# Kernel optimization log

Measured on AMD Instinct MI355X. Metric: run time of the kernel, lower is better.

Reference implementation:

```python
import jax, jax.numpy as jnp
import numpy as np

N = 50000      # nodes
E = 800000     # edges
H = 128        # hidden_features
EF = 8         # edge_features (before distance concat)
L = 2          # num_layers
NF = 100.0     # normalization_factor
NC = 1.0       # norm_constant
ATTN = True
USE_TANH = False
TANH_RANGE = 15.0
EIN = 2 * H + EF + 1  # GCL / coord-MLP edge input dim


def setup_inputs() -> dict:
    key = jax.random.key(0)
    ks = jax.random.split(key, 16)
    s = 0.02
    w = lambda k, shape: (jax.random.normal(k, shape, jnp.float32) * s)
    return dict(
        x=jax.random.normal(ks[0], (N, H), jnp.float32),
        pos=jax.random.normal(ks[1], (N, 3), jnp.float32),
        mask=jnp.ones((N, 1), jnp.float32),
        edge_attr=jax.random.normal(ks[2], (E, EF), jnp.float32),
        edge_index=jax.random.randint(ks[3], (2, E), 0, N),
        # GCL layer params, stacked over L layers
        W_e1=w(ks[4], (L, EIN, H)), b_e1=jnp.zeros((L, H), jnp.float32),
        W_e2=w(ks[5], (L, H, H)),  b_e2=jnp.zeros((L, H), jnp.float32),
        W_att=w(ks[6], (L, H, 1)), b_att=jnp.zeros((L, 1), jnp.float32),
        W_n1=w(ks[7], (L, 2 * H, H)), b_n1=jnp.zeros((L, H), jnp.float32),
        W_n2=w(ks[8], (L, H, H)),  b_n2=jnp.zeros((L, H), jnp.float32),
        # Equivariant coordinate-update MLP (last layer has no bias)
        cW1=w(ks[9], (EIN, H)), cb1=jnp.zeros((H,), jnp.float32),
        cW2=w(ks[10], (H, H)), cb2=jnp.zeros((H,), jnp.float32),
        cW3=w(ks[11], (H, 1)),
    )


def reference(x, pos, mask, edge_attr, edge_index,
              W_e1, b_e1, W_e2, b_e2, W_att, b_att, W_n1, b_n1, W_n2, b_n2,
              cW1, cb1, cW2, cb2, cW3):
    silu = jax.nn.silu
    row, col = edge_index[0], edge_index[1]  # aggregate messages at row
    diff = pos[row] - pos[col]                         # [E, 3]
    d2 = jnp.sum(diff * diff, axis=-1, keepdims=True)  # [E, 1] squared distance
    ea = jnp.concatenate([d2, edge_attr], axis=-1)     # [E, EF+1]

    # GCL message-passing layers (residual node update)
    for l in range(L):
        he = jnp.concatenate([x[row], x[col], ea], axis=-1)   # [E, EIN]
        m = silu(silu(he @ W_e1[l] + b_e1[l]) @ W_e2[l] + b_e2[l])
        if ATTN:
            m = m * jax.nn.sigmoid(m @ W_att[l] + b_att[l])
        agg = jax.ops.segment_sum(m, row, num_segments=N) / NF
        x = x + silu(jnp.concatenate([x, agg], axis=-1) @ W_n1[l] + b_n1[l]) @ W_n2[l] + b_n2[l]

    # Equivariant coordinate update
    he = jnp.concatenate([x[row], x[col], ea], axis=-1)
    phi = silu(silu(he @ cW1 + cb1) @ cW2 + cb2) @ cW3        # [E, 1]
    if USE_TANH:
        phi = jnp.tanh(phi) * TANH_RANGE
    nd = diff / (jnp.sqrt(d2) + NC)                           # normalized direction
    trans = nd * phi                                          # [E, 3]
    pos = pos + (jax.ops.segment_sum(trans, row, num_segments=N) / NF) * mask
    return (x, pos)
```

## Files before the change

kernel.cpp:

```cpp
#include <hip/hip_runtime.h>
#include <hip/hip_bf16.h>
#include <stdint.h>

#define NN 50000
#define NE 800000
#define HH 128

typedef __bf16 bf16x8 __attribute__((ext_vector_type(8)));
typedef float  f32x4  __attribute__((ext_vector_type(4)));
typedef long   f8frag;

__device__ __forceinline__ unsigned short f2bf(float f) {
  union { float f; uint32_t u; } v; v.f = f;
  uint32_t r = v.u + 0x7FFFu + ((v.u >> 16) & 1u);
  return (unsigned short)(r >> 16);
}
__device__ __forceinline__ float b2f(unsigned short u) {
  union { float f; uint32_t u; } v; v.u = (uint32_t)u << 16; return v.f;
}
#if __has_builtin(__builtin_amdgcn_cvt_pk_bf16_f32)
typedef __bf16 bf16x2 __attribute__((ext_vector_type(2)));
__device__ __forceinline__ uint32_t pack2bf(float a, float b) {
  union { bf16x2 v; uint32_t u; } t;
  t.v = __builtin_amdgcn_cvt_pk_bf16_f32(a, b);
  return t.u;
}
#else
__device__ __forceinline__ uint32_t pack2bf(float a, float b) {
  return (uint32_t)f2bf(a) | ((uint32_t)f2bf(b) << 16);
}
#endif
__device__ __forceinline__ uint8_t f2fp8(float v) {
  return (uint8_t)(__builtin_amdgcn_cvt_pk_fp8_f32(v, 0.f, 0, false) & 0xff);
}
__device__ __forceinline__ float silu_f(float x) {
  return x * __builtin_amdgcn_rcpf(1.f + __expf(-x));
}
__device__ __forceinline__ float sigm_f(float x) {
  return __builtin_amdgcn_rcpf(1.f + __expf(-x));
}

__device__ __forceinline__ bf16x8 frag_ld(const short* blk, int row, int q) {
  int c = q ^ ((row >> 1) & 3);
  return *(const bf16x8*)(blk + row * 32 + c * 8);
}
__device__ __forceinline__ int wfrag_off(int row, int q) {
  return row * 32 + ((q ^ ((row >> 1) & 3)) * 8);
}
__device__ __forceinline__ bf16x8 fragf32(const float* src, float sc) {
  float4 lo = *(const float4*)src;
  float4 hi = *(const float4*)(src + 4);
  union { uint32_t u[4]; bf16x8 v; } t;
  t.u[0] = pack2bf(lo.x * sc, lo.y * sc);
  t.u[1] = pack2bf(lo.z * sc, lo.w * sc);
  t.u[2] = pack2bf(hi.x * sc, hi.y * sc);
  t.u[3] = pack2bf(hi.z * sc, hi.w * sc);
  return t.v;
}

__global__ void k_prep_weights(const float* We1, const float* We2, const float* Wn1,
                               const float* Wn2, const float* cW1, const float* cW2,
                               uint8_t* W1f8, short* W2sw, short* Wn1sw, short* Wn2sw,
                               short* W1csw) {
  int idx = blockIdx.x * 256 + threadIdx.x;
  if (idx < 110592) {
    int l = idx / 36864, rem = idx % 36864;
    const float* s = (l == 0) ? We1 : (l == 1) ? We1 + 33920 : cW1;
    int kkb = rem >> 12, r2 = rem & 4095;
    int n = r2 >> 5, kw = r2 & 31;
    int k = kkb * 32 + kw;
    float v = (k < 265) ? s[k * 128 + n] : 0.f;
    W1f8[idx] = f2fp8(v);
    return;
  }
  idx -= 110592;
  if (idx < 49152) {
    int l = idx >> 14, rem = idx & 16383;
    const float* s = (l == 0) ? We2 : (l == 1) ? We2 + 16384 : cW2;
    int kkb = rem >> 12, r2 = rem & 4095, n = r2 >> 5, kw = r2 & 31;
    int cp = kw >> 3, j = kw & 7, c = cp ^ ((n >> 1) & 3);
    int k = kkb * 32 + c * 8 + j;
    W2sw[(l << 14) + (rem)] = (short)f2bf(s[k * 128 + n]);
    return;
  }
  idx -= 49152;
  if (idx < 65536) {
    int l = idx >> 15, rem = idx & 32767;
    const float* s = Wn1 + l * 32768;
    int kkb = rem >> 12, r2 = rem & 4095, n = r2 >> 5, kw = r2 & 31;
    int cp = kw >> 3, j = kw & 7, c = cp ^ ((n >> 1) & 3);
    int k = kkb * 32 + c * 8 + j;
    Wn1sw[(l << 15) + rem] = (short)f2bf(s[k * 128 + n]);
    return;
  }
  idx -= 65536;
  if (idx < 32768) {
    int l = idx >> 14, rem = idx & 16383;
    const float* s = Wn2 + l * 16384;
    int kkb = rem >> 12, r2 = rem & 4095, n = r2 >> 5, kw = r2 & 31;
    int cp = kw >> 3, j = kw & 7, c = cp ^ ((n >> 1) & 3);
    int k = kkb * 32 + c * 8 + j;
    Wn2sw[(l << 14) + rem] = (short)f2bf(s[k * 128 + n]);
    return;
  }
  idx -= 32768;
  if (idx < 98304) {
    int l = idx / 32768, rem = idx % 32768;
    const float* s = (l == 0) ? We1 : (l == 1) ? We1 + 33920 : cW1;
    int kkb = rem >> 13, r2 = rem & 8191, n = r2 >> 5, kw = r2 & 31;
    int cp = kw >> 3, j = kw & 7, c = cp ^ ((n >> 1) & 3);
    int k = kkb * 32 + c * 8 + j;
    float v = (n < 128) ? s[k * 128 + n] : s[(128 + k) * 128 + (n - 128)];
    W1csw[l * 32768 + rem] = (short)f2bf(v);
  }
}

__global__ void k_edge_pre(const float* __restrict__ pos, const float* __restrict__ eattr,
                           const int* __restrict__ ei, const int* __restrict__ inv,
                           int* __restrict__ rowS, int* __restrict__ colS,
                           uint8_t* __restrict__ eaF8, float* __restrict__ ndS) {
  int e = blockIdx.x * 256 + threadIdx.x;
  if (e >= NE) return;
  int r = ei[e], c = ei[NE + e];
  float dx = pos[r * 3 + 0] - pos[c * 3 + 0];
  float dy = pos[r * 3 + 1] - pos[c * 3 + 1];
  float dz = pos[r * 3 + 2] - pos[c * 3 + 2];
  float d2 = dx * dx + dy * dy + dz * dz;
  float invd = __builtin_amdgcn_rcpf(sqrtf(d2) + 1.f);
  int p = inv[e];
  rowS[p] = r;
  colS[p] = c;
  ndS[p * 3 + 0] = dx * invd;
  ndS[p * 3 + 1] = dy * invd;
  ndS[p * 3 + 2] = dz * invd;
  const float* ea = eattr + (size_t)e * 8;
  uint32_t w0 = __builtin_amdgcn_cvt_pk_fp8_f32(d2, ea[0], 0, false);
  w0 = __builtin_amdgcn_cvt_pk_fp8_f32(ea[1], ea[2], w0, true);
  uint32_t w1 = __builtin_amdgcn_cvt_pk_fp8_f32(ea[3], ea[4], 0, false);
  w1 = __builtin_amdgcn_cvt_pk_fp8_f32(ea[5], ea[6], w1, true);
  uint32_t w2 = __builtin_amdgcn_cvt_pk_fp8_f32(ea[7], 0.f, 0, false);
  uint4 v = {w0, w1, w2, 0u};
  *(uint4*)(eaF8 + (size_t)p * 16) = v;
}
__global__ void k_pos_final(const float* __restrict__ pos, const float* __restrict__ mask,
                            const float* __restrict__ pagg, float* __restrict__ out) {
  int i = blockIdx.x * 256 + threadIdx.x;
  if (i < NN * 3) out[i] = pos[i] + pagg[i] * 0.01f * mask[i / 3];
}

__global__ void k_hist(const int* __restrict__ ei, int* __restrict__ cnt) {
  int e = blockIdx.x * 256 + threadIdx.x;
  if (e < NE) atomicAdd(&cnt[ei[e]], 1);
}
__global__ void k_scan_block(const int* __restrict__ cnt, int* __restrict__ offs,
                             int* __restrict__ bsum) {
  __shared__ int s[256];
  int i = blockIdx.x * 256 + threadIdx.x;
  int v = (i < NN) ? cnt[i] : 0;
  s[threadIdx.x] = v;
  __syncthreads();
#pragma unroll
  for (int d = 1; d < 256; d <<= 1) {
    int t = (threadIdx.x >= d) ? s[threadIdx.x - d] : 0;
    __syncthreads();
    s[threadIdx.x] += t;
    __syncthreads();
  }
  if (i < NN) offs[i] = s[threadIdx.x] - v;
  if (threadIdx.x == 255) bsum[blockIdx.x] = s[255];
}
__global__ void k_scan_top(int* __restrict__ bsum) {
  __shared__ int s[256];
  int v = (threadIdx.x < 196) ? bsum[threadIdx.x] : 0;
  s[threadIdx.x] = v;
  __syncthreads();
#pragma unroll
  for (int d = 1; d < 256; d <<= 1) {
    int t = (threadIdx.x >= d) ? s[threadIdx.x - d] : 0;
    __syncthreads();
    s[threadIdx.x] += t;
    __syncthreads();
  }
  if (threadIdx.x < 196) bsum[threadIdx.x] = s[threadIdx.x] - v;
}
__global__ void k_scan_add(int* __restrict__ offs, const int* __restrict__ bsum) {
  int i = blockIdx.x * 256 + threadIdx.x;
  if (i < NN) offs[i] += bsum[blockIdx.x];
}
__global__ void k_scatter(const int* __restrict__ ei, int* __restrict__ offs,
                          int* __restrict__ inv) {
  int e = blockIdx.x * 256 + threadIdx.x;
  if (e < NE) inv[e] = atomicAdd(&offs[ei[e]], 1);
}

__global__ __launch_bounds__(256) void k_h1(
    const float* __restrict__ x, const short* __restrict__ W1c,
    const float* __restrict__ b1, short* __restrict__ H1RC) {
  const int tid = threadIdx.x, lane = tid & 63, w = tid >> 6;
  const int ln = lane & 15, q = lane >> 4;
  const int tile = blockIdx.x;
  size_t nbase[4];
  int wofs[4];
#pragma unroll
  for (int i = 0; i < 4; ++i) {
    int node = tile * 64 + i * 16 + ln;
    nbase[i] = (size_t)(node < NN ? node : (NN - 1)) * 128;
    int row = w * 64 + i * 16 + ln;
    wofs[i] = row * 32 + ((q ^ ((row >> 1) & 3)) * 8);
  }
  f32x4 acc[4][4];
  const f32x4 zero4 = {0.f, 0.f, 0.f, 0.f};
#pragma unroll
  for (int mi = 0; mi < 4; ++mi)
#pragma unroll
    for (int ni = 0; ni < 4; ++ni) acc[mi][ni] = zero4;
#pragma unroll
  for (int kk = 0; kk < 4; ++kk) {
    bf16x8 af[4], bfr[4];
#pragma unroll
    for (int i = 0; i < 4; ++i) af[i] = fragf32(x + nbase[i] + kk * 32 + q * 8, 1.f);
#pragma unroll
    for (int i = 0; i < 4; ++i) bfr[i] = *(const bf16x8*)(W1c + kk * 8192 + wofs[i]);
#pragma unroll
    for (int mi = 0; mi < 4; ++mi)
#pragma unroll
      for (int ni = 0; ni < 4; ++ni)
        acc[mi][ni] = __builtin_amdgcn_mfma_f32_16x16x32_bf16(af[mi], bfr[ni], acc[mi][ni], 0, 0, 0);
  }
  float b1v[4];
#pragma unroll
  for (int ni = 0; ni < 4; ++ni) {
    int ch = w * 64 + ni * 16 + ln;
    b1v[ni] = (ch < 128) ? b1[ch] : 0.f;
  }
#pragma unroll
  for (int mi = 0; mi < 4; ++mi)
#pragma unroll
    for (int r = 0; r < 4; ++r) {
      int node = tile * 64 + mi * 16 + q * 4 + r;
      if (node < NN) {
        ushort4 pk;
        pk.x = f2bf(acc[mi][0][r] + b1v[0]);
        pk.y = f2bf(acc[mi][1][r] + b1v[1]);
        pk.z = f2bf(acc[mi][2][r] + b1v[2]);
        pk.w = f2bf(acc[mi][3][r] + b1v[3]);
        *(ushort4*)(H1RC + (size_t)node * 256 + w * 64 + ln * 4) = pk;
      }
    }
}

template <int COORD>
__global__ __launch_bounds__(256, 4) void k_edge_gemm(
    const short* __restrict__ H1RC, const uint8_t* __restrict__ eaF8,
    const int* __restrict__ rowS, const int* __restrict__ colS,
    const uint8_t* __restrict__ W1f8, const short* __restrict__ W2l,
    const float* __restrict__ b2,
    const float* __restrict__ wred, const float* __restrict__ batt,
    const float* __restrict__ ndS, float* outAcc) {
  __shared__ __align__(16) short A2s[8192];
  __shared__ float redp[64][2];
  __shared__ __align__(16) unsigned short attb[64];
  __shared__ int srow[64];
  __shared__ __align__(8) unsigned char srunS[64];
  __shared__ int runrowS[64];
  __shared__ int cntS[1];

  const int tid = threadIdx.x;
  const int lane = tid & 63;
  const int w = tid >> 6;
  const int ln = lane & 15, q = lane >> 4;
  const int wm = w >> 1, wn = w & 1;

  const int nwg = gridDim.x;
  const int qq = nwg >> 3, rr = nwg & 7;
  const int xcd = blockIdx.x & 7, bidx = blockIdx.x >> 3;
  const int tile = (xcd < rr ? xcd * (qq + 1) : rr * (qq + 1) + (xcd - rr) * qq) + bidx;

  if (tid < 64) srow[tid] = rowS[tile * 64 + tid];
  __syncthreads();

  bool is_start = (tid < 64) && (tid == 0 || srow[tid] != srow[tid - 1]);
  unsigned long long bmask = __ballot(is_start);
  if (tid == 0) cntS[0] = __popcll(bmask);
  if (tid < 64) {
    int run = __popcll(bmask & ((1ull << lane) - 1ull)) + (is_start ? 1 : 0) - 1;
    srunS[tid] = (unsigned char)run;
    if (is_start) runrowS[run] = srow[tid];
  }

  const int e0 = wm * 32 + ln, e1 = e0 + 16;
  const uint32_t cbp = (uint32_t)(wn * 64 + q * 16);
  const uint32_t hr0 = (uint32_t)srow[e0] * 256u + cbp;
  const uint32_t hr1 = (uint32_t)srow[e1] * 256u + cbp;
  const uint32_t hc0 = (uint32_t)colS[tile * 64 + e0] * 256u + 128u + cbp;
  const uint32_t hc1 = (uint32_t)colS[tile * 64 + e1] * 256u + 128u + cbp;
  const uint32_t ea0 = (uint32_t)(tile * 64 + e0) * 16u + (uint32_t)((q & 1) * 8);
  const uint32_t ea1 = (uint32_t)(tile * 64 + e1) * 16u + (uint32_t)((q & 1) * 8);
  int wofs8[4], wofs[4];
#pragma unroll
  for (int i = 0; i < 4; ++i) {
    wofs8[i] = (wn * 64 + i * 16 + ln) * 32 + q * 8;
    wofs[i] = wfrag_off(wn * 64 + i * 16 + ln, q);
  }

  union U8 { uint4 v; unsigned short s[8]; };
  U8 xr[2][2], xc[2][2];
  xr[0][0].v = *(const uint4*)(H1RC + hr0);
  xr[0][1].v = *(const uint4*)(H1RC + hr0 + 8);
  xr[1][0].v = *(const uint4*)(H1RC + hr1);
  xr[1][1].v = *(const uint4*)(H1RC + hr1 + 8);
  xc[0][0].v = *(const uint4*)(H1RC + hc0);
  xc[0][1].v = *(const uint4*)(H1RC + hc0 + 8);
  xc[1][0].v = *(const uint4*)(H1RC + hc1);
  xc[1][1].v = *(const uint4*)(H1RC + hc1 + 8);

  f32x4 acc[4][2];
  const f32x4 zero4 = {0.f, 0.f, 0.f, 0.f};
#pragma unroll
  for (int ni = 0; ni < 4; ++ni)
#pragma unroll
    for (int mi = 0; mi < 2; ++mi) acc[ni][mi] = zero4;

  {
    const uint8_t* W1ea = W1f8 + 8 * 4096;
    f8frag wf[4], hf[2];
#pragma unroll
    for (int i = 0; i < 4; ++i) wf[i] = *(const f8frag*)(W1ea + wofs8[i]);
    hf[0] = (q < 2) ? *(const f8frag*)(eaF8 + ea0) : 0L;
    hf[1] = (q < 2) ? *(const f8frag*)(eaF8 + ea1) : 0L;
#pragma unroll
    for (int ni = 0; ni < 4; ++ni)
#pragma unroll
      for (int mi = 0; mi < 2; ++mi)
        acc[ni][mi] = __builtin_amdgcn_mfma_f32_16x16x32_fp8_fp8(wf[ni], hf[mi], acc[ni][mi], 0, 0, 0);
  }

#pragma unroll
  for (int ni = 0; ni < 4; ++ni) {
    int cb = wn * 64 + ni * 16 + q * 4;
    int kkb = cb >> 5, cc = (cb >> 3) & 3, j0 = cb & 7;
#pragma unroll
    for (int mi = 0; mi < 2; ++mi) {
      int edge = wm * 32 + mi * 16 + ln;
      int addr = kkb * 2048 + edge * 32 + ((cc ^ ((edge >> 1) & 3)) * 8) + j0;
      float h0 = silu_f(acc[ni][mi][0] + b2f(xr[mi][0].s[ni]) + b2f(xc[mi][0].s[ni]));
      float h1 = silu_f(acc[ni][mi][1] + b2f(xr[mi][0].s[4 + ni]) + b2f(xc[mi][0].s[4 + ni]));
      float h2 = silu_f(acc[ni][mi][2] + b2f(xr[mi][1].s[ni]) + b2f(xc[mi][1].s[ni]));
      float h3 = silu_f(acc[ni][mi][3] + b2f(xr[mi][1].s[4 + ni]) + b2f(xc[mi][1].s[4 + ni]));
      uint2 pk;
      pk.x = pack2bf(h0, h1);
      pk.y = pack2bf(h2, h3);
      *(uint2*)(A2s + addr) = pk;
    }
  }
  __syncthreads();

  f32x4 acc2[4][2];
#pragma unroll
  for (int ni = 0; ni < 4; ++ni)
#pragma unroll
    for (int mi = 0; mi < 2; ++mi) acc2[ni][mi] = zero4;
#pragma unroll
  for (int kk = 0; kk < 4; ++kk) {
    bf16x8 wf[4], hf[2];
#pragma unroll
    for (int i = 0; i < 4; ++i) wf[i] = *(const bf16x8*)(W2l + kk * 4096 + wofs[i]);
#pragma unroll
    for (int i = 0; i < 2; ++i) hf[i] = frag_ld(A2s + kk * 2048, wm * 32 + i * 16 + ln, q);
#pragma unroll
    for (int ni = 0; ni < 4; ++ni)
#pragma unroll
      for (int mi = 0; mi < 2; ++mi)
        acc2[ni][mi] = __builtin_amdgcn_mfma_f32_16x16x32_bf16(wf[ni], hf[mi], acc2[ni][mi], 0, 0, 0);
  }

  float4 b2v[4], wv[4];
#pragma unroll
  for (int ni = 0; ni < 4; ++ni) {
    b2v[ni] = *(const float4*)(b2 + wn * 64 + ni * 16 + q * 4);
    wv[ni]  = *(const float4*)(wred + wn * 64 + ni * 16 + q * 4);
  }
  float p[2] = {0.f, 0.f};
#pragma unroll
  for (int ni = 0; ni < 4; ++ni)
#pragma unroll
    for (int mi = 0; mi < 2; ++mi)
#pragma unroll
      for (int r = 0; r < 4; ++r) {
        float v = silu_f(acc2[ni][mi][r] + ((const float*)&b2v[ni])[r]);
        acc2[ni][mi][r] = v;
        p[mi] += v * ((const float*)&wv[ni])[r];
      }
#pragma unroll
  for (int mi = 0; mi < 2; ++mi) {
    p[mi] += __shfl_xor(p[mi], 16, 64);
    p[mi] += __shfl_xor(p[mi], 32, 64);
  }
  if (lane < 16) {
#pragma unroll
    for (int mi = 0; mi < 2; ++mi) redp[wm * 32 + mi * 16 + ln][wn] = p[mi];
  }
  __syncthreads();

  if (COORD == 0) {
    if (tid < 64) attb[tid] = f2bf(sigm_f(redp[tid][0] + redp[tid][1] + batt[0]));
#pragma unroll
    for (int ni = 0; ni < 4; ++ni)
#pragma unroll
      for (int mi = 0; mi < 2; ++mi) {
        int eb = mi * 16 + ln;
        int cE = (eb >> 3) & 3, jE = eb & 7;
#pragma unroll
        for (int r = 0; r < 4; ++r) {
          int chan2 = wn * 64 + ni * 16 + q * 4 + r;
          int addr = wm * 4096 + chan2 * 32 + ((cE ^ ((chan2 >> 1) & 3)) * 8) + jE;
          union { float f; uint32_t u; } vv;
          vv.f = acc2[ni][mi][r];
          A2s[addr] = (short)((vv.u + 0x8000u) >> 16);
        }
      }
    __syncthreads();
    const int nruns = cntS[0];
    bf16x8 bfrg[2][2];
#pragma unroll
    for (int kk = 0; kk < 2; ++kk)
#pragma unroll
      for (int ni = 0; ni < 2; ++ni)
        bfrg[kk][ni] = frag_ld(A2s + kk * 4096, w * 32 + ni * 16 + ln, q);
    const int npass = (nruns + 15) >> 4;
    for (int pp = 0; pp < npass; ++pp) {
      const unsigned int base = pp * 16;
      f32x4 a3c[2] = {zero4, zero4};
#pragma unroll
      for (int kk = 0; kk < 2; ++kk) {
        uint2 sb = *(const uint2*)(srunS + kk * 32 + q * 8);
        U8 ab;
        ab.v = *(const uint4*)(attb + kk * 32 + q * 8);
        union { short s[8]; bf16x8 v; } af;
#pragma unroll
        for (int j = 0; j < 4; ++j)
          af.s[j] = (((sb.x >> (8 * j)) & 255u) == base + (unsigned)ln) ? (short)ab.s[j] : (short)0;
#pragma unroll
        for (int j = 0; j < 4; ++j)
          af.s[4 + j] = (((sb.y >> (8 * j)) & 255u) == base + (unsigned)ln) ? (short)ab.s[4 + j] : (short)0;
        a3c[0] = __builtin_amdgcn_mfma_f32_16x16x32_bf16(af.v, bfrg[kk][0], a3c[0], 0, 0, 0);
        a3c[1] = __builtin_amdgcn_mfma_f32_16x16x32_bf16(af.v, bfrg[kk][1], a3c[1], 0, 0, 0);
      }
#pragma unroll
      for (int ni = 0; ni < 2; ++ni)
#pragma unroll
        for (int r = 0; r < 4; ++r) {
          int run = (int)base + q * 4 + r;
          if (run < nruns) {
            int rw = runrowS[run];
            atomicAdd(&outAcc[(size_t)rw * 128 + (w * 32 + ni * 16 + ln)], a3c[ni][r]);
          }
        }
    }
  } else {
    float* ndl = (float*)A2s;
    if (tid < 64) {
      float phi = redp[tid][0] + redp[tid][1];
      ndl[tid * 3 + 0] = ndS[(size_t)(tile * 64 + tid) * 3 + 0] * phi;
      ndl[tid * 3 + 1] = ndS[(size_t)(tile * 64 + tid) * 3 + 1] * phi;
      ndl[tid * 3 + 2] = ndS[(size_t)(tile * 64 + tid) * 3 + 2] * phi;
    }
    __syncthreads();
    if (is_start) {
      int myrow = srow[tid];
      float s0 = 0.f, s1 = 0.f, s2 = 0.f;
      for (int j = tid; j < 64 && srow[j] == myrow; ++j) {
        s0 += ndl[j * 3 + 0];
        s1 += ndl[j * 3 + 1];
        s2 += ndl[j * 3 + 2];
      }
      atomicAdd(&outAcc[myrow * 3 + 0], s0);
      atomicAdd(&outAcc[myrow * 3 + 1], s1);
      atomicAdd(&outAcc[myrow * 3 + 2], s2);
    }
  }
}

__global__ __launch_bounds__(256) void k_node_gemm(
    const float* __restrict__ agg,
    const short* __restrict__ Wn1l, const short* __restrict__ Wn2l,
    const float* __restrict__ b1, const float* __restrict__ b2,
    const float* __restrict__ xres, float* __restrict__ xout,
    const short* __restrict__ W1cN, const float* __restrict__ b1N,
    short* __restrict__ H1RC) {
  __shared__ short A2s[4 * 2048];

  const int tid = threadIdx.x;
  const int lane = tid & 63;
  const int w = tid >> 6;
  const int ln = lane & 15, q = lane >> 4;
  const int wm = w >> 1, wn = w & 1;
  const int tile = blockIdx.x;

  size_t nbase[2];
  int wofs[4];
#pragma unroll
  for (int i = 0; i < 2; ++i) {
    int node = tile * 64 + wm * 32 + i * 16 + ln;
    nbase[i] = (size_t)(node < NN ? node : (NN - 1)) * 128;
  }
#pragma unroll
  for (int i = 0; i < 4; ++i) wofs[i] = wfrag_off(wn * 64 + i * 16 + ln, q);

  f32x4 acc[2][4];
  const f32x4 zero4 = {0.f, 0.f, 0.f, 0.f};
#pragma unroll
  for (int mi = 0; mi < 2; ++mi)
#pragma unroll
    for (int ni = 0; ni < 4; ++ni) acc[mi][ni] = zero4;

#pragma unroll
  for (int kk = 0; kk < 8; ++kk) {
    bf16x8 af[2], bfr[4];
#pragma unroll
    for (int i = 0; i < 2; ++i) {
      if (kk < 4) af[i] = fragf32(xres + nbase[i] + kk * 32 + q * 8, 1.f);
      else        af[i] = fragf32(agg + nbase[i] + (kk - 4) * 32 + q * 8, 0.01f);
    }
#pragma unroll
    for (int i = 0; i < 4; ++i) bfr[i] = *(const bf16x8*)(Wn1l + kk * 4096 + wofs[i]);
#pragma unroll
    for (int mi = 0; mi < 2; ++mi)
#pragma unroll
      for (int ni = 0; ni < 4; ++ni)
        acc[mi][ni] = __builtin_amdgcn_mfma_f32_16x16x32_bf16(af[mi], bfr[ni], acc[mi][ni], 0, 0, 0);
  }

  float b1v[4];
#pragma unroll
  for (int ni = 0; ni < 4; ++ni) b1v[ni] = b1[wn * 64 + ni * 16 + ln];
#pragma unroll
  for (int mi = 0; mi < 2; ++mi)
#pragma unroll
    for (int ni = 0; ni < 4; ++ni) {
      int chan = wn * 64 + ni * 16 + ln;
      int kkb = chan >> 5, c = (chan >> 3) & 3, jj = chan & 7;
#pragma unroll
      for (int r = 0; r < 4; ++r) {
        int m = wm * 32 + mi * 16 + q * 4 + r;
        float v = silu_f(acc[mi][ni][r] + b1v[ni]);
        A2s[kkb * 2048 + m * 32 + ((c ^ ((m >> 1) & 3)) * 8) + jj] = (short)f2bf(v);
      }
    }
  __syncthreads();

  f32x4 acc2[2][4];
#pragma unroll
  for (int mi = 0; mi < 2; ++mi)
#pragma unroll
    for (int ni = 0; ni < 4; ++ni) acc2[mi][ni] = zero4;
#pragma unroll
  for (int kk = 0; kk < 4; ++kk) {
    bf16x8 af[2], bfr[4];
#pragma unroll
    for (int i = 0; i < 2; ++i) af[i] = frag_ld(A2s + kk * 2048, wm * 32 + i * 16 + ln, q);
#pragma unroll
    for (int i = 0; i < 4; ++i) bfr[i] = *(const bf16x8*)(Wn2l + kk * 4096 + wofs[i]);
#pragma unroll
    for (int mi = 0; mi < 2; ++mi)
#pragma unroll
      for (int ni = 0; ni < 4; ++ni)
        acc2[mi][ni] = __builtin_amdgcn_mfma_f32_16x16x32_bf16(af[mi], bfr[ni], acc2[mi][ni], 0, 0, 0);
  }

  float b2v[4];
#pragma unroll
  for (int ni = 0; ni < 4; ++ni) b2v[ni] = b2[wn * 64 + ni * 16 + ln];
#pragma unroll
  for (int mi = 0; mi < 2; ++mi)
#pragma unroll
    for (int r = 0; r < 4; ++r) {
      int m = wm * 32 + mi * 16 + q * 4 + r;
      int node = tile * 64 + m;
      if (node < NN) {
#pragma unroll
        for (int ni = 0; ni < 4; ++ni) {
          int chan = wn * 64 + ni * 16 + ln;
          float v = acc2[mi][ni][r] + b2v[ni] + xres[(size_t)node * 128 + chan];
          acc2[mi][ni][r] = v;
          xout[(size_t)node * 128 + chan] = v;
        }
      }
    }

  __syncthreads();
#pragma unroll
  for (int mi = 0; mi < 2; ++mi)
#pragma unroll
    for (int ni = 0; ni < 4; ++ni) {
      int chan = wn * 64 + ni * 16 + ln;
      int kkb = chan >> 5, c = (chan >> 3) & 3, jj = chan & 7;
#pragma unroll
      for (int r = 0; r < 4; ++r) {
        int m = wm * 32 + mi * 16 + q * 4 + r;
        A2s[kkb * 2048 + m * 32 + ((c ^ ((m >> 1) & 3)) * 8) + jj] = (short)f2bf(acc2[mi][ni][r]);
      }
    }
  __syncthreads();

  int wofsH[4];
#pragma unroll
  for (int i = 0; i < 4; ++i) {
    int row = w * 64 + i * 16 + ln;
    wofsH[i] = row * 32 + ((q ^ ((row >> 1) & 3)) * 8);
  }
  f32x4 acc3[4][4];
#pragma unroll
  for (int mi = 0; mi < 4; ++mi)
#pragma unroll
    for (int ni = 0; ni < 4; ++ni) acc3[mi][ni] = zero4;
#pragma unroll
  for (int kk = 0; kk < 4; ++kk) {
    bf16x8 af[4], bfr[4];
#pragma unroll
    for (int i = 0; i < 4; ++i) af[i] = frag_ld(A2s + kk * 2048, i * 16 + ln, q);
#pragma unroll
    for (int i = 0; i < 4; ++i) bfr[i] = *(const bf16x8*)(W1cN + kk * 8192 + wofsH[i]);
#pragma unroll
    for (int mi = 0; mi < 4; ++mi)
#pragma unroll
      for (int ni = 0; ni < 4; ++ni)
        acc3[mi][ni] = __builtin_amdgcn_mfma_f32_16x16x32_bf16(af[mi], bfr[ni], acc3[mi][ni], 0, 0, 0);
  }
  float b1v2[4];
#pragma unroll
  for (int ni = 0; ni < 4; ++ni) {
    int ch = w * 64 + ni * 16 + ln;
    b1v2[ni] = (ch < 128) ? b1N[ch] : 0.f;
  }
#pragma unroll
  for (int mi = 0; mi < 4; ++mi)
#pragma unroll
    for (int r = 0; r < 4; ++r) {
      int node = tile * 64 + mi * 16 + q * 4 + r;
      if (node < NN) {
        ushort4 pk;
        pk.x = f2bf(acc3[mi][0][r] + b1v2[0]);
        pk.y = f2bf(acc3[mi][1][r] + b1v2[1]);
        pk.z = f2bf(acc3[mi][2][r] + b1v2[2]);
        pk.w = f2bf(acc3[mi][3][r] + b1v2[3]);
        *(ushort4*)(H1RC + (size_t)node * 256 + w * 64 + ln * 4) = pk;
      }
    }
}

extern "C" void kernel_launch(void* const* d_in, const int* in_sizes, int n_in,
                              void* d_out, int out_size, void* d_ws, size_t ws_size,
                              hipStream_t stream) {
  const float* x    = (const float*)d_in[0];
  const float* pos  = (const float*)d_in[1];
  const float* mask = (const float*)d_in[2];
  const float* eattr= (const float*)d_in[3];
  const int*   ei   = (const int*)d_in[4];
  const float* We1  = (const float*)d_in[5];
  const float* be1  = (const float*)d_in[6];
  const float* We2  = (const float*)d_in[7];
  const float* be2  = (const float*)d_in[8];
  const float* Watt = (const float*)d_in[9];
  const float* batt = (const float*)d_in[10];
  const float* Wn1  = (const float*)d_in[11];
  const float* bn1  = (const float*)d_in[12];
  const float* Wn2  = (const float*)d_in[13];
  const float* bn2  = (const float*)d_in[14];
  const float* cW1  = (const float*)d_in[15];
  const float* cb1  = (const float*)d_in[16];
  const float* cW2  = (const float*)d_in[17];
  const float* cb2  = (const float*)d_in[18];
  const float* cW3  = (const float*)d_in[19];

  char* p = (char*)d_ws;
  auto carve = [&](size_t bytes) { char* r = p; p += (bytes + 511) & ~(size_t)511; return r; };
  short*   H1RC  = (short*)carve((size_t)NN * 256 * 2);
  uint8_t* eaF8  = (uint8_t*)carve((size_t)NE * 16 + 256);
  int*     rowS  = (int*)carve((size_t)NE * 4);
  int*     colS  = (int*)carve((size_t)NE * 4);
  float*   ndS   = (float*)carve((size_t)NE * 3 * 4);
  float*   agg   = (float*)carve((size_t)NN * 128 * 4);
  float*   xcur  = (float*)carve((size_t)NN * 128 * 4);
  float*   pagg  = (float*)carve((size_t)NN * 3 * 4);
  uint8_t* W1f8  = (uint8_t*)carve(3 * 36864);
  short*   W2sw  = (short*)carve(3 * 16384 * 2);
  short*   Wn1sw = (short*)carve(2 * 32768 * 2);
  short*   Wn2sw = (short*)carve(2 * 16384 * 2);
  short*   W1csw = (short*)carve(3 * 32768 * 2);
  int*     cnt   = (int*)carve((size_t)NN * 4);
  int*     offs  = (int*)carve((size_t)NN * 4);
  int*     bsum  = (int*)carve(256 * 4);
  int*     inv   = (int*)carve((size_t)NE * 4);

  float* xout_f = (float*)d_out;
  float* pout_f = xout_f + NN * 128;

  k_prep_weights<<<1392, 256, 0, stream>>>(We1, We2, Wn1, Wn2, cW1, cW2,
                                           W1f8, W2sw, Wn1sw, Wn2sw, W1csw);

  hipMemsetAsync(cnt, 0, (size_t)NN * 4, stream);
  k_hist<<<3125, 256, 0, stream>>>(ei, cnt);
  k_scan_block<<<196, 256, 0, stream>>>(cnt, offs, bsum);
  k_scan_top<<<1, 256, 0, stream>>>(bsum);
  k_scan_add<<<196, 256, 0, stream>>>(offs, bsum);
  k_scatter<<<3125, 256, 0, stream>>>(ei, offs, inv);
  k_edge_pre<<<3125, 256, 0, stream>>>(pos, eattr, ei, inv, rowS, colS, eaF8, ndS);

  k_h1<<<782, 256, 0, stream>>>(x, W1csw, be1, H1RC);

  hipMemsetAsync(agg, 0, (size_t)NN * 128 * 4, stream);
  k_edge_gemm<0><<<12500, 256, 0, stream>>>(H1RC, eaF8, rowS, colS,
      W1f8, W2sw, be2, Watt, batt, (const float*)nullptr, agg);
  k_node_gemm<<<782, 256, 0, stream>>>(agg, Wn1sw, Wn2sw, bn1, bn2,
      x, xcur, W1csw + 32768, be1 + 128, H1RC);

  hipMemsetAsync(agg, 0, (size_t)NN * 128 * 4, stream);
  k_edge_gemm<0><<<12500, 256, 0, stream>>>(H1RC, eaF8, rowS, colS,
      W1f8 + 36864, W2sw + 16384, be2 + 128, Watt + 128, batt + 1,
      (const float*)nullptr, agg);
  k_node_gemm<<<782, 256, 0, stream>>>(agg, Wn1sw + 32768, Wn2sw + 16384,
      bn1 + 128, bn2 + 128, xcur, xout_f, W1csw + 2 * 32768, cb1, H1RC);

  hipMemsetAsync(pagg, 0, (size_t)NN * 3 * 4, stream);
  k_edge_gemm<1><<<12500, 256, 0, stream>>>(H1RC, eaF8, rowS, colS,
      W1f8 + 2 * 36864, W2sw + 2 * 16384, cb2, cW3, (const float*)nullptr, ndS, pagg);
  k_pos_final<<<587, 256, 0, stream>>>(pos, mask, pagg, pout_f);
}
```

Measured before the change: 712.2 us.

## Fuse agg zeroing into node kernels, gather-style edge prep, raise edge occupancy

The two memsets of the aggregation buffer are replaced by zero stores inside k_h1 and the first k_node_gemm, each block clearing its own tile right after its reads of agg. The scatter kernel now writes a sorted-to-original edge index, so edge_pre reads in scattered order but writes the sorted arrays contiguously instead of scattering them. k_edge_gemm drops one block-wide barrier by reading row indices directly from global memory, and its launch bound goes from 4 to 5 blocks per unit. The risks are more register pressure or spills at the higher occupancy target, and the in-kernel zeroing depends on each block's agg reads finishing before its own zero stores.

```diff
diff --git a/kernel.cpp b/kernel.cpp
--- a/kernel.cpp
+++ b/kernel.cpp
@@ -116,18 +116,18 @@
 }
 
 __global__ void k_edge_pre(const float* __restrict__ pos, const float* __restrict__ eattr,
-                           const int* __restrict__ ei, const int* __restrict__ inv,
+                           const int* __restrict__ ei, const int* __restrict__ sortedIdx,
                            int* __restrict__ rowS, int* __restrict__ colS,
                            uint8_t* __restrict__ eaF8, float* __restrict__ ndS) {
-  int e = blockIdx.x * 256 + threadIdx.x;
-  if (e >= NE) return;
+  int p = blockIdx.x * 256 + threadIdx.x;
+  if (p >= NE) return;
+  int e = sortedIdx[p];
   int r = ei[e], c = ei[NE + e];
   float dx = pos[r * 3 + 0] - pos[c * 3 + 0];
   float dy = pos[r * 3 + 1] - pos[c * 3 + 1];
   float dz = pos[r * 3 + 2] - pos[c * 3 + 2];
   float d2 = dx * dx + dy * dy + dz * dz;
   float invd = __builtin_amdgcn_rcpf(sqrtf(d2) + 1.f);
-  int p = inv[e];
   rowS[p] = r;
   colS[p] = c;
   ndS[p * 3 + 0] = dx * invd;
@@ -188,17 +188,27 @@
   if (i < NN) offs[i] += bsum[blockIdx.x];
 }
 __global__ void k_scatter(const int* __restrict__ ei, int* __restrict__ offs,
-                          int* __restrict__ inv) {
+                          int* __restrict__ sortedIdx) {
   int e = blockIdx.x * 256 + threadIdx.x;
-  if (e < NE) inv[e] = atomicAdd(&offs[ei[e]], 1);
+  if (e < NE) sortedIdx[atomicAdd(&offs[ei[e]], 1)] = e;
 }
 
 __global__ __launch_bounds__(256) void k_h1(
     const float* __restrict__ x, const short* __restrict__ W1c,
-    const float* __restrict__ b1, short* __restrict__ H1RC) {
+    const float* __restrict__ b1, short* __restrict__ H1RC,
+    float* __restrict__ aggZ) {
   const int tid = threadIdx.x, lane = tid & 63, w = tid >> 6;
   const int ln = lane & 15, q = lane >> 4;
   const int tile = blockIdx.x;
+  {
+    float4* a4 = (float4*)aggZ;
+    const float4 z4 = {0.f, 0.f, 0.f, 0.f};
+#pragma unroll
+    for (int k = 0; k < 8; ++k) {
+      int i4 = tile * 2048 + k * 256 + tid;
+      if (i4 < NN * 32) a4[i4] = z4;
+    }
+  }
   size_t nbase[4];
   int wofs[4];
 #pragma unroll
@@ -250,7 +260,7 @@
 }
 
 template <int COORD>
-__global__ __launch_bounds__(256, 4) void k_edge_gemm(
+__global__ __launch_bounds__(256, 5) void k_edge_gemm(
     const short* __restrict__ H1RC, const uint8_t* __restrict__ eaF8,
     const int* __restrict__ rowS, const int* __restrict__ colS,
     const uint8_t* __restrict__ W1f8, const short* __restrict__ W2l,
@@ -275,27 +285,29 @@
   const int qq = nwg >> 3, rr = nwg & 7;
   const int xcd = blockIdx.x & 7, bidx = blockIdx.x >> 3;
   const int tile = (xcd < rr ? xcd * (qq + 1) : rr * (qq + 1) + (xcd - rr) * qq) + bidx;
-
-  if (tid < 64) srow[tid] = rowS[tile * 64 + tid];
-  __syncthreads();
-
-  bool is_start = (tid < 64) && (tid == 0 || srow[tid] != srow[tid - 1]);
-  unsigned long long bmask = __ballot(is_start);
-  if (tid == 0) cntS[0] = __popcll(bmask);
-  if (tid < 64) {
+  const int ebase = tile * 64;
+
+  bool is_start = false;
+  if (w == 0) {
+    int myrow = rowS[ebase + tid];
+    srow[tid] = myrow;
+    int prevrow = (tid > 0) ? rowS[ebase + tid - 1] : (myrow ^ 1);
+    is_start = (tid == 0) || (myrow != prevrow);
+    unsigned long long bmask = __ballot(is_start);
+    if (tid == 0) cntS[0] = __popcll(bmask);
     int run = __popcll(bmask & ((1ull << lane) - 1ull)) + (is_start ? 1 : 0) - 1;
     srunS[tid] = (unsigned char)run;
-    if (is_start) runrowS[run] = srow[tid];
+    if (is_start) runrowS[run] = myrow;
   }
 
   const int e0 = wm * 32 + ln, e1 = e0 + 16;
   const uint32_t cbp = (uint32_t)(wn * 64 + q * 16);
-  const uint32_t hr0 = (uint32_t)srow[e0] * 256u + cbp;
-  const uint32_t hr1 = (uint32_t)srow[e1] * 256u + cbp;
-  const uint32_t hc0 = (uint32_t)colS[tile * 64 + e0] * 256u + 128u + cbp;
-  const uint32_t hc1 = (uint32_t)colS[tile * 64 + e1] * 256u + 128u + cbp;
-  const uint32_t ea0 = (uint32_t)(tile * 64 + e0) * 16u + (uint32_t)((q & 1) * 8);
-  const uint32_t ea1 = (uint32_t)(tile * 64 + e1) * 16u + (uint32_t)((q & 1) * 8);
+  const uint32_t hr0 = (uint32_t)rowS[ebase + e0] * 256u + cbp;
+  const uint32_t hr1 = (uint32_t)rowS[ebase + e1] * 256u + cbp;
+  const uint32_t hc0 = (uint32_t)colS[ebase + e0] * 256u + 128u + cbp;
+  const uint32_t hc1 = (uint32_t)colS[ebase + e1] * 256u + 128u + cbp;
+  const uint32_t ea0 = (uint32_t)(ebase + e0) * 16u + (uint32_t)((q & 1) * 8);
+  const uint32_t ea1 = (uint32_t)(ebase + e1) * 16u + (uint32_t)((q & 1) * 8);
   int wofs8[4], wofs[4];
 #pragma unroll
   for (int i = 0; i < 4; ++i) {
@@ -461,9 +473,9 @@
     float* ndl = (float*)A2s;
     if (tid < 64) {
       float phi = redp[tid][0] + redp[tid][1];
-      ndl[tid * 3 + 0] = ndS[(size_t)(tile * 64 + tid) * 3 + 0] * phi;
-      ndl[tid * 3 + 1] = ndS[(size_t)(tile * 64 + tid) * 3 + 1] * phi;
-      ndl[tid * 3 + 2] = ndS[(size_t)(tile * 64 + tid) * 3 + 2] * phi;
+      ndl[tid * 3 + 0] = ndS[(size_t)(ebase + tid) * 3 + 0] * phi;
+      ndl[tid * 3 + 1] = ndS[(size_t)(ebase + tid) * 3 + 1] * phi;
+      ndl[tid * 3 + 2] = ndS[(size_t)(ebase + tid) * 3 + 2] * phi;
     }
     __syncthreads();
     if (is_start) {
@@ -487,7 +499,7 @@
     const float* __restrict__ b1, const float* __restrict__ b2,
     const float* __restrict__ xres, float* __restrict__ xout,
     const short* __restrict__ W1cN, const float* __restrict__ b1N,
-    short* __restrict__ H1RC) {
+    short* __restrict__ H1RC, float* __restrict__ aggZ) {
   __shared__ short A2s[4 * 2048];
 
   const int tid = threadIdx.x;
@@ -529,6 +541,16 @@
 #pragma unroll
       for (int ni = 0; ni < 4; ++ni)
         acc[mi][ni] = __builtin_amdgcn_mfma_f32_16x16x32_bf16(af[mi], bfr[ni], acc[mi][ni], 0, 0, 0);
+  }
+
+  if (aggZ) {
+    float4* a4 = (float4*)aggZ;
+    const float4 z4 = {0.f, 0.f, 0.f, 0.f};
+#pragma unroll
+    for (int k = 0; k < 8; ++k) {
+      int i4 = tile * 2048 + k * 256 + tid;
+      if (i4 < NN * 32) a4[i4] = z4;
+    }
   }
 
   float b1v[4];
@@ -691,7 +713,7 @@
   int*     cnt   = (int*)carve((size_t)NN * 4);
   int*     offs  = (int*)carve((size_t)NN * 4);
   int*     bsum  = (int*)carve(256 * 4);
-  int*     inv   = (int*)carve((size_t)NE * 4);
+  int*     sortedIdx = (int*)carve((size_t)NE * 4);
 
   float* xout_f = (float*)d_out;
   float* pout_f = xout_f + NN * 128;
@@ -704,23 +726,22 @@
   k_scan_block<<<196, 256, 0, stream>>>(cnt, offs, bsum);
   k_scan_top<<<1, 256, 0, stream>>>(bsum);
   k_scan_add<<<196, 256, 0, stream>>>(offs, bsum);
-  k_scatter<<<3125, 256, 0, stream>>>(ei, offs, inv);
-  k_edge_pre<<<3125, 256, 0, stream>>>(pos, eattr, ei, inv, rowS, colS, eaF8, ndS);
-
-  k_h1<<<782, 256, 0, stream>>>(x, W1csw, be1, H1RC);
-
-  hipMemsetAsync(agg, 0, (size_t)NN * 128 * 4, stream);
+  k_scatter<<<3125, 256, 0, stream>>>(ei, offs, sortedIdx);
+  k_edge_pre<<<3125, 256, 0, stream>>>(pos, eattr, ei, sortedIdx, rowS, colS, eaF8, ndS);
+
+  k_h1<<<782, 256, 0, stream>>>(x, W1csw, be1, H1RC, agg);
+
   k_edge_gemm<0><<<12500, 256, 0, stream>>>(H1RC, eaF8, rowS, colS,
       W1f8, W2sw, be2, Watt, batt, (const float*)nullptr, agg);
   k_node_gemm<<<782, 256, 0, stream>>>(agg, Wn1sw, Wn2sw, bn1, bn2,
-      x, xcur, W1csw + 32768, be1 + 128, H1RC);
-
-  hipMemsetAsync(agg, 0, (size_t)NN * 128 * 4, stream);
+      x, xcur, W1csw + 32768, be1 + 128, H1RC, agg);
+
   k_edge_gemm<0><<<12500, 256, 0, stream>>>(H1RC, eaF8, rowS, colS,
       W1f8 + 36864, W2sw + 16384, be2 + 128, Watt + 128, batt + 1,
       (const float*)nullptr, agg);
   k_node_gemm<<<782, 256, 0, stream>>>(agg, Wn1sw + 32768, Wn2sw + 16384,
-      bn1 + 128, bn2 + 128, xcur, xout_f, W1csw + 2 * 32768, cb1, H1RC);
+      bn1 + 128, bn2 + 128, xcur, xout_f, W1csw + 2 * 32768, cb1, H1RC,
+      (float*)nullptr);
 
   hipMemsetAsync(pagg, 0, (size_t)NN * 3 * 4, stream);
   k_edge_gemm<1><<<12500, 256, 0, stream>>>(H1RC, eaF8, rowS, colS,
```

After: 705.2 us. Within noise of the previous version (-1.0%).
